# Kernel tuning notes

Hardware: AMD Instinct MI355X
Metric: run time of the kernel (lower is better)

The kernel has to match this reference:

```python
import jax, jax.numpy as jnp
import numpy as np

C = 512
C8 = C // 8  # query/key projection dim


def _conv1x1(x, W, b):
    # x: [B,C,H,W], W: [O,C], b: [O] -> [B,O,H,W]
    return jnp.einsum('bchw,oc->bohw', x, W) + b[None, :, None, None]


def setup_inputs() -> dict:
    key = jax.random.key(0)
    ks = jax.random.split(key, 13)
    B, H, Wd = 4, 64, 64
    s = 0.02
    return {
        'x_rgb': jax.random.normal(ks[0], (B, C, H, Wd), jnp.float32),
        'x_dep': jax.random.normal(ks[1], (B, C, H, Wd), jnp.float32),
        'Wq': jax.random.normal(ks[2], (C8, C), jnp.float32) * s,
        'bq': jnp.zeros((C8,), jnp.float32),
        'Wk': jax.random.normal(ks[3], (C8, C), jnp.float32) * s,
        'bk': jnp.zeros((C8,), jnp.float32),
        'Wdq': jax.random.normal(ks[4], (C8, C), jnp.float32) * s,
        'bdq': jnp.zeros((C8,), jnp.float32),
        'Wdk': jax.random.normal(ks[5], (C8, C), jnp.float32) * s,
        'bdk': jnp.zeros((C8,), jnp.float32),
        'Wv': jax.random.normal(ks[6], (C, C), jnp.float32) * s,
        'bv': jnp.zeros((C,), jnp.float32),
        'gamma': jnp.zeros((1,), jnp.float32),
    }


def reference(x_rgb, x_dep, Wq, bq, Wk, bk, Wdq, bdq, Wdk, bdk, Wv, bv, gamma):
    B, Cc, H, Wd = x_rgb.shape
    N = H * Wd
    # 1x1 conv projections, flattened over spatial positions -> [B, c, N]
    q = _conv1x1(x_rgb, Wq, bq).reshape(B, C8, N)
    k = _conv1x1(x_rgb, Wk, bk).reshape(B, C8, N)
    qd = _conv1x1(x_dep, Wdq, bdq).reshape(B, C8, N)
    kd = _conv1x1(x_dep, Wdk, bdk).reshape(B, C8, N)
    # fused dual-stream energy: [B, N, N]
    energy = jnp.einsum('bci,bcj->bij', q, k) + jnp.einsum('bci,bcj->bij', qd, kd)
    attention = jax.nn.softmax(energy, axis=-1)
    v = _conv1x1(x_rgb, Wv, bv).reshape(B, Cc, N)
    # out[b,c,i] = sum_j v[b,c,j] * attention[b,i,j]
    out = jnp.einsum('bcj,bij->bci', v, attention).reshape(B, Cc, H, Wd)
    return gamma[0] * out + x_rgb
```

## Files before the change

### kernel.cpp

```cpp
#include <hip/hip_runtime.h>
#include <math.h>

#define B_ 4
#define C_ 512
#define D_ 128
#define N_ 4096

typedef short s4v __attribute__((ext_vector_type(4)));
typedef short s8v __attribute__((ext_vector_type(8)));
typedef float f4v __attribute__((ext_vector_type(4)));

__device__ __forceinline__ unsigned short f2bf(float x) {
    union { float f; unsigned u; } v; v.f = x;
    unsigned r = v.u + 0x7FFF + ((v.u >> 16) & 1);
    return (unsigned short)(r >> 16);
}
__device__ __forceinline__ float bf2f(unsigned short h) {
    union { unsigned u; float f; } v; v.u = ((unsigned)h) << 16; return v.f;
}

__global__ __launch_bounds__(256) void cvt_w_kernel(
    const float* __restrict__ Wq,  const float* __restrict__ bq,
    const float* __restrict__ Wk,  const float* __restrict__ bk,
    const float* __restrict__ Wdq, const float* __restrict__ bdq,
    const float* __restrict__ Wdk, const float* __restrict__ bdk,
    const float* __restrict__ Wv,  const float* __restrict__ bv,
    unsigned short* __restrict__ Wb, float* __restrict__ biasb)
{
    int t = blockIdx.x * 256 + threadIdx.x;
    int e0 = t * 8;
    int row = e0 >> 9, c = e0 & 511;
    const float* src; int r0;
    if (row < 64)       { src = Wq;  r0 = row; }
    else if (row < 128) { src = Wk;  r0 = row - 64; }
    else if (row < 640) { src = Wv;  r0 = row - 128; }
    else if (row < 704) { src = Wdq; r0 = row - 640; }
    else                { src = Wdk; r0 = row - 704; }
    const float* p = src + (size_t)r0 * 512 + c;
    s8v o;
    #pragma unroll
    for (int u = 0; u < 8; ++u) ((unsigned short*)&o)[u] = f2bf(p[u]);
    *(s8v*)&Wb[e0] = o;
    if (blockIdx.x == 0) {
        #pragma unroll
        for (int s = 0; s < 3; ++s) {
            int o2 = threadIdx.x + 256 * s;
            float v;
            if (o2 < 64)       v = bq[o2];
            else if (o2 < 128) v = bk[o2 - 64];
            else if (o2 < 640) v = bv[o2 - 128];
            else if (o2 < 704) v = bdq[o2 - 640];
            else               v = bdk[o2 - 704];
            biasb[o2] = v;
        }
    }
}

__global__ __launch_bounds__(256) void xpose_kernel(
    const float* __restrict__ x_rgb, const float* __restrict__ x_dep,
    unsigned short* __restrict__ Xt)
{
    __shared__ __align__(16) unsigned short Ls[64 * 72];
    const int cT = blockIdx.x & 7, iT = blockIdx.x >> 3;
    const int b = blockIdx.y, st = blockIdx.z;
    const int t = threadIdx.x;
    const float* Xb = (st ? x_dep : x_rgb) + (size_t)b * C_ * N_;

    const int c4 = t >> 4, i4 = t & 15;
    {
        const float* xp = Xb + (size_t)(cT * 64 + c4 * 4) * N_ + iT * 64 + i4 * 4;
        float4 r0 = *(const float4*)(xp);
        float4 r1 = *(const float4*)(xp + N_);
        float4 r2 = *(const float4*)(xp + 2 * N_);
        float4 r3 = *(const float4*)(xp + 3 * N_);
        s4v p0 = { (short)f2bf(r0.x), (short)f2bf(r1.x), (short)f2bf(r2.x), (short)f2bf(r3.x) };
        s4v p1 = { (short)f2bf(r0.y), (short)f2bf(r1.y), (short)f2bf(r2.y), (short)f2bf(r3.y) };
        s4v p2 = { (short)f2bf(r0.z), (short)f2bf(r1.z), (short)f2bf(r2.z), (short)f2bf(r3.z) };
        s4v p3 = { (short)f2bf(r0.w), (short)f2bf(r1.w), (short)f2bf(r2.w), (short)f2bf(r3.w) };
        *(s4v*)&Ls[(i4 * 4 + 0) * 72 + c4 * 4] = p0;
        *(s4v*)&Ls[(i4 * 4 + 1) * 72 + c4 * 4] = p1;
        *(s4v*)&Ls[(i4 * 4 + 2) * 72 + c4 * 4] = p2;
        *(s4v*)&Ls[(i4 * 4 + 3) * 72 + c4 * 4] = p3;
    }
    __syncthreads();
    unsigned short* dst = Xt + ((size_t)(st * 4 + b) * N_ + iT * 64) * 512 + cT * 64;
    #pragma unroll
    for (int s = 0; s < 2; ++s) {
        int lin = t + 256 * s;
        int row = lin >> 3, g = lin & 7;
        *(s8v*)&dst[(size_t)row * 512 + g * 8] = *(const s8v*)&Ls[row * 72 + g * 8];
    }
}

__global__ __launch_bounds__(256) void gemm_kernel(
    const unsigned short* __restrict__ Wb, const float* __restrict__ biasb,
    const unsigned short* __restrict__ Xt,
    unsigned short* __restrict__ Q, unsigned short* __restrict__ K,
    unsigned short* __restrict__ V)
{
    __shared__ __align__(16) unsigned short Ws[128 * 64];
    __shared__ __align__(16) unsigned short Xs[128 * 64];
    const int b  = blockIdx.x >> 5;
    const int i0 = (blockIdx.x & 31) * 128;
    const int by = blockIdx.y;
    const int mbase = by * 128;
    const int st = (by == 5);
    const int t = threadIdx.x, w = t >> 6;
    const int lane = t & 63, col = lane & 15, quad = lane >> 4;
    const int mh = (w & 1) * 64, nh = (w >> 1) * 64;

    const unsigned short* Wg = Wb + (size_t)mbase * 512;
    const unsigned short* Xg = Xt + ((size_t)(st * 4 + b) * N_ + i0) * 512;

    f4v acc[4][4];
    #pragma unroll
    for (int mt = 0; mt < 4; ++mt)
        #pragma unroll
        for (int nt = 0; nt < 4; ++nt) acc[mt][nt] = (f4v){0.f, 0.f, 0.f, 0.f};

    for (int kc = 0; kc < 8; ++kc) {
        const int k0 = kc * 64;
        s8v wt[4], xt[4];
        #pragma unroll
        for (int s = 0; s < 4; ++s) {
            int lin = t + 256 * s;
            int row = lin >> 3, g = lin & 7;
            wt[s] = *(const s8v*)&Wg[(size_t)row * 512 + k0 + g * 8];
            xt[s] = *(const s8v*)&Xg[(size_t)row * 512 + k0 + g * 8];
        }
        __syncthreads();
        #pragma unroll
        for (int s = 0; s < 4; ++s) {
            int lin = t + 256 * s;
            int row = lin >> 3, g = lin & 7;
            int soff = row * 64 + ((g ^ (row & 7)) * 8);
            *(s8v*)&Ws[soff] = wt[s];
            *(s8v*)&Xs[soff] = xt[s];
        }
        __syncthreads();
        #pragma unroll
        for (int kk = 0; kk < 2; ++kk) {
            const int gq = kk * 4 + quad;
            s8v af[4], bf[4];
            #pragma unroll
            for (int mt = 0; mt < 4; ++mt) {
                int r = mh + mt * 16 + col;
                af[mt] = *(const s8v*)&Ws[r * 64 + ((gq ^ (r & 7)) * 8)];
            }
            #pragma unroll
            for (int nt = 0; nt < 4; ++nt) {
                int r = nh + nt * 16 + col;
                bf[nt] = *(const s8v*)&Xs[r * 64 + ((gq ^ (r & 7)) * 8)];
            }
            #pragma unroll
            for (int nt = 0; nt < 4; ++nt)
                #pragma unroll
                for (int mt = 0; mt < 4; ++mt)
                    acc[mt][nt] = __builtin_amdgcn_mfma_f32_16x16x32_bf16(
                        af[mt], bf[nt], acc[mt][nt], 0, 0, 0);
        }
    }

    const int mlo0 = mbase + mh;
    #pragma unroll
    for (int mt = 0; mt < 4; ++mt) {
        const int mlo = mlo0 + mt * 16;
        f4v bi = *(const f4v*)&biasb[mlo + quad * 4];
        if (mlo < 128 || mlo >= 640) {
            unsigned short* dst; int dbase;
            if (mlo < 64)       { dst = Q; dbase = mlo; }
            else if (mlo < 128) { dst = K; dbase = mlo - 64; }
            else if (mlo < 704) { dst = Q; dbase = 64 + (mlo - 640); }
            else                { dst = K; dbase = 64 + (mlo - 704); }
            #pragma unroll
            for (int nt = 0; nt < 4; ++nt) {
                int i = i0 + nh + nt * 16 + col;
                s4v pk = { (short)f2bf(acc[mt][nt][0] + bi[0]),
                           (short)f2bf(acc[mt][nt][1] + bi[1]),
                           (short)f2bf(acc[mt][nt][2] + bi[2]),
                           (short)f2bf(acc[mt][nt][3] + bi[3]) };
                *(s4v*)&dst[((size_t)b * N_ + i) * D_ + dbase + quad * 4] = pk;
            }
        } else {
            int c0 = mlo - 128 + quad * 4;
            #pragma unroll
            for (int nt = 0; nt < 4; ++nt) {
                int i = i0 + nh + nt * 16 + col;
                #pragma unroll
                for (int r = 0; r < 4; ++r)
                    V[((size_t)b * C_ + c0 + r) * N_ + i] =
                        f2bf(acc[mt][nt][r] + bi[r]);
            }
        }
    }
}

__global__ __launch_bounds__(256, 2) void attn_kernel(
    const unsigned short* __restrict__ Q, const unsigned short* __restrict__ K,
    const unsigned short* __restrict__ V,
    unsigned short* __restrict__ O_ws, float* __restrict__ l_ws)
{
    __shared__ __align__(16) unsigned short Ks[32 * 136];
    __shared__ __align__(16) unsigned short Ps[64 * 40];
    __shared__ __align__(16) unsigned short Vs[512 * 32];
    __shared__ float lred[2][64];

    const int b  = blockIdx.y;
    const int i0 = blockIdx.x * 64;
    const int jh = blockIdx.z;
    const int jb = jh * 2048;
    const int t = threadIdx.x, w = t >> 6;
    const int lane = t & 63, col = lane & 15, quad = lane >> 4;
    const int ih = w & 1, jq = w >> 1;

    const unsigned short* Kg = K + (size_t)b * N_ * D_;
    const unsigned short* Vg = V + (size_t)b * C_ * N_;

    s8v qf[2][4];
    #pragma unroll
    for (int ig = 0; ig < 2; ++ig) {
        const unsigned short* qr =
            Q + ((size_t)b * N_ + i0 + ih * 32 + ig * 16 + col) * D_ + quad * 8;
        #pragma unroll
        for (int kk = 0; kk < 4; ++kk) qf[ig][kk] = *(const s8v*)(qr + kk * 32);
    }

    f4v accO[4][8];
    #pragma unroll
    for (int rt = 0; rt < 4; ++rt)
        #pragma unroll
        for (int ct = 0; ct < 8; ++ct) accO[rt][ct] = (f4v){0.f, 0.f, 0.f, 0.f};
    float lsum[2] = {0.f, 0.f};

    for (int tt = 0; tt < 64; ++tt) {
        const int j0 = jb + tt * 32;
        s8v kt[2], vt[8];
        #pragma unroll
        for (int s = 0; s < 2; ++s) {
            int gi = t + 256 * s;
            kt[s] = *(const s8v*)&Kg[(size_t)(j0 + (gi >> 4)) * D_ + (gi & 15) * 8];
        }
        #pragma unroll
        for (int s = 0; s < 8; ++s) {
            int gi = t + 256 * s;
            vt[s] = *(const s8v*)&Vg[(size_t)(gi >> 2) * N_ + j0 + (gi & 3) * 8];
        }
        __syncthreads();
        #pragma unroll
        for (int s = 0; s < 2; ++s) {
            int gi = t + 256 * s;
            *(s8v*)&Ks[(gi >> 4) * 136 + (gi & 15) * 8] = kt[s];
        }
        #pragma unroll
        for (int s = 0; s < 8; ++s) {
            int gi = t + 256 * s;
            int c = gi >> 2, g = gi & 3;
            int sw = (g + c + (c >> 2)) & 3;
            *(s8v*)&Vs[c * 32 + sw * 8] = vt[s];
        }
        __syncthreads();
        f4v s0 = (f4v){0.f, 0.f, 0.f, 0.f};
        f4v s1 = (f4v){0.f, 0.f, 0.f, 0.f};
        #pragma unroll
        for (int kk = 0; kk < 4; ++kk) {
            s8v kf = *(const s8v*)&Ks[(jq * 16 + col) * 136 + kk * 32 + quad * 8];
            s0 = __builtin_amdgcn_mfma_f32_16x16x32_bf16(kf, qf[0][kk], s0, 0, 0, 0);
            s1 = __builtin_amdgcn_mfma_f32_16x16x32_bf16(kf, qf[1][kk], s1, 0, 0, 0);
        }
        #pragma unroll
        for (int ig = 0; ig < 2; ++ig) {
            f4v sv = ig ? s1 : s0;
            s4v p; float ls = 0.f;
            #pragma unroll
            for (int r = 0; r < 4; ++r) {
                float e = __expf(sv[r]);
                ls += e;
                p[r] = (short)f2bf(e);
            }
            lsum[ig] += ls;
            *(s4v*)&Ps[(ih * 32 + ig * 16 + col) * 40 + jq * 16 + quad * 4] = p;
        }
        __syncthreads();
        s8v pf[4];
        #pragma unroll
        for (int rt = 0; rt < 4; ++rt)
            pf[rt] = *(const s8v*)&Ps[(rt * 16 + col) * 40 + quad * 8];
        #pragma unroll
        for (int ct = 0; ct < 8; ++ct) {
            int row = w * 128 + ct * 16 + col;
            int sw = (quad + row + (row >> 2)) & 3;
            s8v vf = *(const s8v*)&Vs[row * 32 + sw * 8];
            #pragma unroll
            for (int rt = 0; rt < 4; ++rt)
                accO[rt][ct] = __builtin_amdgcn_mfma_f32_16x16x32_bf16(pf[rt], vf, accO[rt][ct], 0, 0, 0);
        }
    }

    #pragma unroll
    for (int ig = 0; ig < 2; ++ig) {
        float v = lsum[ig];
        v += __shfl_xor(v, 16);
        v += __shfl_xor(v, 32);
        if (quad == 0) lred[jq][ih * 32 + ig * 16 + col] = v;
    }
    __syncthreads();
    if (t < 64)
        l_ws[((size_t)jh * B_ + b) * N_ + i0 + t] = lred[0][t] + lred[1][t];

    const size_t wbase =
        ((((size_t)jh * B_ + b) * 64 + blockIdx.x) * 4 + w) * 8192;
    #pragma unroll
    for (int ct = 0; ct < 8; ++ct)
        #pragma unroll
        for (int rt = 0; rt < 4; ++rt) {
            s4v pk = { (short)f2bf(accO[rt][ct][0]), (short)f2bf(accO[rt][ct][1]),
                       (short)f2bf(accO[rt][ct][2]), (short)f2bf(accO[rt][ct][3]) };
            *(s4v*)&O_ws[wbase + (size_t)(ct * 4 + rt) * 256 + lane * 4] = pk;
        }
}

__global__ __launch_bounds__(256) void combine_kernel(
    const unsigned short* __restrict__ O_ws, const float* __restrict__ l_ws,
    const float* __restrict__ x_rgb, const float* __restrict__ gamma,
    float* __restrict__ out)
{
    const size_t half = (size_t)B_ * 64 * 4 * 8192;
    int idx = blockIdx.x * 256 + threadIdx.x;
    int i4 = idx & 1023;
    int c  = (idx >> 10) & 511;
    int b  = idx >> 19;
    int i  = i4 * 4;
    int i0b = i >> 6, il = i & 63;
    int rt = il >> 4, qd = (il >> 2) & 3;
    int w = c >> 7, cl = c & 127, ct = cl >> 4, col = cl & 15;
    size_t obase = (((size_t)b * 64 + i0b) * 4 + w) * 8192
                 + (size_t)(ct * 4 + rt) * 256 + (qd * 16 + col) * 4;
    s4v o0 = *(const s4v*)&O_ws[obase];
    s4v o1 = *(const s4v*)&O_ws[half + obase];
    float4 l0 = *(const float4*)&l_ws[(size_t)b * N_ + i];
    float4 l1 = *(const float4*)&l_ws[(size_t)(B_ + b) * N_ + i];
    size_t base = ((size_t)b * C_ + c) * N_ + i;
    float4 x4 = *(const float4*)&x_rgb[base];
    float g = gamma[0];
    float4 r;
    r.x = g * (bf2f((unsigned short)o0[0]) + bf2f((unsigned short)o1[0])) / (l0.x + l1.x) + x4.x;
    r.y = g * (bf2f((unsigned short)o0[1]) + bf2f((unsigned short)o1[1])) / (l0.y + l1.y) + x4.y;
    r.z = g * (bf2f((unsigned short)o0[2]) + bf2f((unsigned short)o1[2])) / (l0.z + l1.z) + x4.z;
    r.w = g * (bf2f((unsigned short)o0[3]) + bf2f((unsigned short)o1[3])) / (l0.w + l1.w) + x4.w;
    *(float4*)&out[base] = r;
}

extern "C" void kernel_launch(void* const* d_in, const int* in_sizes, int n_in,
                              void* d_out, int out_size, void* d_ws, size_t ws_size,
                              hipStream_t stream) {
    (void)in_sizes; (void)n_in; (void)out_size; (void)ws_size;
    const float* x_rgb = (const float*)d_in[0];
    const float* x_dep = (const float*)d_in[1];
    const float* Wq    = (const float*)d_in[2];
    const float* bq    = (const float*)d_in[3];
    const float* Wk    = (const float*)d_in[4];
    const float* bk    = (const float*)d_in[5];
    const float* Wdq   = (const float*)d_in[6];
    const float* bdq   = (const float*)d_in[7];
    const float* Wdk   = (const float*)d_in[8];
    const float* bdk   = (const float*)d_in[9];
    const float* Wv    = (const float*)d_in[10];
    const float* bv    = (const float*)d_in[11];
    const float* gamma = (const float*)d_in[12];
    float* out = (float*)d_out;

    unsigned short* Q     = (unsigned short*)d_ws;
    unsigned short* K     = Q + (size_t)B_ * N_ * D_;
    unsigned short* V     = K + (size_t)B_ * N_ * D_;
    unsigned short* Wb    = V + (size_t)B_ * C_ * N_;
    float*          biasb = (float*)(Wb + 768 * 512);
    unsigned short* XtO   = (unsigned short*)(biasb + 1024);
    float*          l_ws  = (float*)(XtO + (size_t)2 * B_ * C_ * N_);

    cvt_w_kernel<<<dim3(192), 256, 0, stream>>>(
        Wq, bq, Wk, bk, Wdq, bdq, Wdk, bdk, Wv, bv, Wb, biasb);
    xpose_kernel<<<dim3(512, 4, 2), 256, 0, stream>>>(x_rgb, x_dep, XtO);
    gemm_kernel<<<dim3(128, 6), 256, 0, stream>>>(Wb, biasb, XtO, Q, K, V);
    attn_kernel<<<dim3(64, 4, 2), 256, 0, stream>>>(Q, K, V, XtO, l_ws);
    combine_kernel<<<dim3(8192), 256, 0, stream>>>(XtO, l_ws, x_rgb, gamma, out);
}
```

Measured before the change: 291.8 us.

## Double-buffer K tile in LDS and load V fragments directly from global

Each wave now reads its V MFMA operands straight from global memory into registers instead of staging the whole 512x32 V tile through LDS. The K tile is double-buffered in shared memory, with the next tile prefetched while the current one is used. This cuts the per-iteration barrier count from three to one and removes the V LDS traffic. In exchange, every wave does its own strided global V reads, which rely on L2/L1 reuse and may be less coalesced, and register pressure rises with 8 V fragments live.

```diff
diff --git a/kernel.cpp b/kernel.cpp
--- a/kernel.cpp
+++ b/kernel.cpp
@@ -200,9 +200,8 @@
     const unsigned short* __restrict__ V,
     unsigned short* __restrict__ O_ws, float* __restrict__ l_ws)
 {
-    __shared__ __align__(16) unsigned short Ks[32 * 136];
-    __shared__ __align__(16) unsigned short Ps[64 * 40];
-    __shared__ __align__(16) unsigned short Vs[512 * 32];
+    __shared__ __align__(16) unsigned short Ks[2][32 * 136];
+    __shared__ __align__(16) unsigned short Ps[2][64 * 40];
     __shared__ float lred[2][64];
 
     const int b  = blockIdx.y;
@@ -232,38 +231,38 @@
         for (int ct = 0; ct < 8; ++ct) accO[rt][ct] = (f4v){0.f, 0.f, 0.f, 0.f};
     float lsum[2] = {0.f, 0.f};
 
+    const unsigned short* Vt = Vg + (size_t)(w * 128 + col) * N_ + quad * 8;
+
+    #pragma unroll
+    for (int s = 0; s < 2; ++s) {
+        int gi = t + 256 * s;
+        s8v k0v = *(const s8v*)&Kg[(size_t)(jb + (gi >> 4)) * D_ + (gi & 15) * 8];
+        *(s8v*)&Ks[0][(gi >> 4) * 136 + (gi & 15) * 8] = k0v;
+    }
+    __syncthreads();
+
     for (int tt = 0; tt < 64; ++tt) {
+        const int cur = tt & 1;
         const int j0 = jb + tt * 32;
-        s8v kt[2], vt[8];
-        #pragma unroll
-        for (int s = 0; s < 2; ++s) {
-            int gi = t + 256 * s;
-            kt[s] = *(const s8v*)&Kg[(size_t)(j0 + (gi >> 4)) * D_ + (gi & 15) * 8];
-        }
-        #pragma unroll
-        for (int s = 0; s < 8; ++s) {
-            int gi = t + 256 * s;
-            vt[s] = *(const s8v*)&Vg[(size_t)(gi >> 2) * N_ + j0 + (gi & 3) * 8];
-        }
-        __syncthreads();
-        #pragma unroll
-        for (int s = 0; s < 2; ++s) {
-            int gi = t + 256 * s;
-            *(s8v*)&Ks[(gi >> 4) * 136 + (gi & 15) * 8] = kt[s];
-        }
-        #pragma unroll
-        for (int s = 0; s < 8; ++s) {
-            int gi = t + 256 * s;
-            int c = gi >> 2, g = gi & 3;
-            int sw = (g + c + (c >> 2)) & 3;
-            *(s8v*)&Vs[c * 32 + sw * 8] = vt[s];
-        }
-        __syncthreads();
+
+        s8v kt[2];
+        if (tt < 63) {
+            #pragma unroll
+            for (int s = 0; s < 2; ++s) {
+                int gi = t + 256 * s;
+                kt[s] = *(const s8v*)&Kg[(size_t)(j0 + 32 + (gi >> 4)) * D_ + (gi & 15) * 8];
+            }
+        }
+        s8v vf[8];
+        #pragma unroll
+        for (int ct = 0; ct < 8; ++ct)
+            vf[ct] = *(const s8v*)(Vt + (size_t)(ct * 16) * N_ + j0);
+
         f4v s0 = (f4v){0.f, 0.f, 0.f, 0.f};
         f4v s1 = (f4v){0.f, 0.f, 0.f, 0.f};
         #pragma unroll
         for (int kk = 0; kk < 4; ++kk) {
-            s8v kf = *(const s8v*)&Ks[(jq * 16 + col) * 136 + kk * 32 + quad * 8];
+            s8v kf = *(const s8v*)&Ks[cur][(jq * 16 + col) * 136 + kk * 32 + quad * 8];
             s0 = __builtin_amdgcn_mfma_f32_16x16x32_bf16(kf, qf[0][kk], s0, 0, 0, 0);
             s1 = __builtin_amdgcn_mfma_f32_16x16x32_bf16(kf, qf[1][kk], s1, 0, 0, 0);
         }
@@ -278,22 +277,26 @@
                 p[r] = (short)f2bf(e);
             }
             lsum[ig] += ls;
-            *(s4v*)&Ps[(ih * 32 + ig * 16 + col) * 40 + jq * 16 + quad * 4] = p;
+            *(s4v*)&Ps[cur][(ih * 32 + ig * 16 + col) * 40 + jq * 16 + quad * 4] = p;
+        }
+        if (tt < 63) {
+            #pragma unroll
+            for (int s = 0; s < 2; ++s) {
+                int gi = t + 256 * s;
+                *(s8v*)&Ks[cur ^ 1][(gi >> 4) * 136 + (gi & 15) * 8] = kt[s];
+            }
         }
         __syncthreads();
         s8v pf[4];
         #pragma unroll
         for (int rt = 0; rt < 4; ++rt)
-            pf[rt] = *(const s8v*)&Ps[(rt * 16 + col) * 40 + quad * 8];
-        #pragma unroll
-        for (int ct = 0; ct < 8; ++ct) {
-            int row = w * 128 + ct * 16 + col;
-            int sw = (quad + row + (row >> 2)) & 3;
-            s8v vf = *(const s8v*)&Vs[row * 32 + sw * 8];
+            pf[rt] = *(const s8v*)&Ps[cur][(rt * 16 + col) * 40 + quad * 8];
+        #pragma unroll
+        for (int ct = 0; ct < 8; ++ct)
             #pragma unroll
             for (int rt = 0; rt < 4; ++rt)
-                accO[rt][ct] = __builtin_amdgcn_mfma_f32_16x16x32_bf16(pf[rt], vf, accO[rt][ct], 0, 0, 0);
-        }
+                accO[rt][ct] = __builtin_amdgcn_mfma_f32_16x16x32_bf16(
+                    pf[rt], vf[ct], accO[rt][ct], 0, 0, 0);
     }
 
     #pragma unroll
```

Measured after the change: 316.8 us. 1.09x slower.
